# Kernel optimization log

Measured on AMD Instinct MI355X. Metric: run time of the kernel, lower is better.

The kernel has to match this reference:

```python
import jax, jax.numpy as jnp
import numpy as np

D_MODEL = 1024
N_HEADS = 16
D_K = D_MODEL // N_HEADS


def _xavier(key, shape):
    fan_in, fan_out = shape[1], shape[0]
    a = np.sqrt(6.0 / (fan_in + fan_out))
    return jax.random.uniform(key, shape, jnp.float32, -a, a)


def setup_inputs() -> dict:
    key = jax.random.key(0)
    kx, kq, kk, kv, ko = jax.random.split(key, 5)
    x = jax.random.normal(kx, (2, 2048, D_MODEL), jnp.float32)
    # nn.Linear weights are [out, in]; y = x @ W.T
    Wq = _xavier(kq, (D_MODEL, D_MODEL))
    Wk = _xavier(kk, (D_MODEL, D_MODEL))
    Wv = _xavier(kv, (D_MODEL, D_MODEL))
    Wo = _xavier(ko, (D_MODEL, D_MODEL))
    bo = jnp.zeros((D_MODEL,), jnp.float32)
    return {"x": x, "Wq": Wq, "Wk": Wk, "Wv": Wv, "Wo": Wo, "bo": bo}


def reference(x, Wq, Wk, Wv, Wo, bo):
    B, S, D = x.shape
    def split_heads(t):
        # [B,S,D] -> [B,H,S,d_k]
        return t.reshape(B, S, N_HEADS, D_K).transpose(0, 2, 1, 3)
    Q = split_heads(x @ Wq.T)
    K = split_heads(x @ Wk.T)
    V = split_heads(x @ Wv.T)
    scale = 1.0 / jnp.sqrt(jnp.asarray(D_K, x.dtype))
    scores = jnp.einsum('bhqd,bhkd->bhqk', Q, K) * scale  # [B,H,S,S]
    attn = jax.nn.softmax(scores, axis=-1)
    out = jnp.einsum('bhqk,bhkd->bhqd', attn, V)  # [B,H,S,d_k]
    out = out.transpose(0, 2, 1, 3).reshape(B, S, D)  # merge heads
    return out @ Wo.T + bo
```

## Files before the change

### kernel.cpp

```cpp
#include <hip/hip_runtime.h>


typedef __attribute__((ext_vector_type(8))) short bf16x8;
typedef __attribute__((ext_vector_type(4))) short bf16x4;
typedef __attribute__((ext_vector_type(4))) float f32x4;
typedef __attribute__((ext_vector_type(2))) unsigned int u32x2;

#define GK 1024
#define SEQ 2048
#define NHEAD 16
#define DKD 64
#define PADW 72

#define MFMA32(a, b, c) __builtin_amdgcn_mfma_f32_16x16x32_bf16((a), (b), (c), 0, 0, 0)

#if __has_builtin(__builtin_amdgcn_mfma_f32_16x16x16bf16_1k)
#define HAVE_MFMA16 1
#define MFMA16(a, b, c) __builtin_amdgcn_mfma_f32_16x16x16bf16_1k((a), (b), (c), 0, 0, 0)
#else
#define HAVE_MFMA16 0
#endif

#if __has_builtin(__builtin_amdgcn_exp2f)
#define EXP2(x) __builtin_amdgcn_exp2f(x)
#else
#define EXP2(x) exp2f(x)
#endif

#define QSCALE 0.18033688011f

static __device__ __forceinline__ unsigned short f2bf(float f) {
    unsigned int u = __float_as_uint(f);
    u += 0x7fffu + ((u >> 16) & 1u);
    return (unsigned short)(u >> 16);
}

static __device__ __forceinline__ unsigned int pack_bf2(float a, float b) {
    unsigned int ua = __float_as_uint(a) + 0x8000u;
    unsigned int ub = __float_as_uint(b) + 0x8000u;
    return __builtin_amdgcn_perm(ub, ua, 0x07060302u);
}

__global__ __launch_bounds__(256) void cast_all(const float* __restrict__ x,
                                                const float* __restrict__ wq,
                                                const float* __restrict__ wk,
                                                const float* __restrict__ wv,
                                                const float* __restrict__ wo,
                                                unsigned short* __restrict__ Xb,
                                                unsigned short* __restrict__ Wqkv,
                                                unsigned short* __restrict__ Wob) {
    const int bid = blockIdx.x;
    const float* src; unsigned short* dst; int off;
    if (bid < 4096)      { src = x;  dst = Xb;             off = bid; }
    else if (bid < 5120) { src = wq; dst = Wqkv;           off = bid - 4096; }
    else if (bid < 6144) { src = wk; dst = Wqkv + 1048576; off = bid - 5120; }
    else if (bid < 7168) { src = wv; dst = Wqkv + 2097152; off = bid - 6144; }
    else                 { src = wo; dst = Wob;            off = bid - 7168; }
    const int i = off * 1024 + threadIdx.x * 4;
    float4 v = *(const float4*)(src + i);
    u32x2 p; p.x = pack_bf2(v.x, v.y); p.y = pack_bf2(v.z, v.w);
    *(u32x2*)(dst + i) = p;
}

template <int MODE, int BN>
__global__ __launch_bounds__(256) void gemm_bt(const unsigned short* __restrict__ A,
                                               const unsigned short* __restrict__ Bw,
                                               unsigned short* __restrict__ outb,
                                               float* __restrict__ outf,
                                               const float* __restrict__ bias) {
    constexpr int NJ = BN / 32;
    __shared__ __align__(16) unsigned short As[128 * 32];
    __shared__ __align__(16) unsigned short Bs[BN * 32];
    __shared__ __align__(16) unsigned short E[(MODE == 0) ? 4 * 64 * PADW : 4];

    const int t    = threadIdx.x;
    const int lane = t & 63;
    const int w    = t >> 6;
    const int wm   = (w >> 1) * 64;
    const int wn   = (w & 1) * (BN / 2);
    const int bm0  = blockIdx.x * 128;
    const int bn0  = blockIdx.y * BN;
    const int lm   = lane & 15;
    const int lq   = lane >> 4;
    const int kc   = lq * 8;

    const unsigned short* Ab = A + (size_t)bm0 * GK;
    const unsigned short* Bb = Bw + (size_t)bn0 * GK;

    f32x4 acc[4][NJ];
#pragma unroll
    for (int i = 0; i < 4; i++)
#pragma unroll
        for (int j = 0; j < NJ; j++) acc[i][j] = (f32x4){0.f, 0.f, 0.f, 0.f};

    const int q_uni = (t & ~63);

    for (int k0 = 0; k0 < GK; k0 += 32) {
        __syncthreads();
#pragma unroll
        for (int i = 0; i < 2; ++i) {
            int q = i * 256 + t;
            int r = q >> 2;
            int c = (q & 3) * 8;
            int q0 = i * 256 + q_uni;
            __builtin_amdgcn_global_load_lds(
                (const __attribute__((address_space(1))) void*)(Ab + (size_t)r * GK + k0 + c),
                (__attribute__((address_space(3))) void*)(As + (size_t)q0 * 8),
                16, 0, 0);
        }
#pragma unroll
        for (int i = 0; i < BN / 64; ++i) {
            int q = i * 256 + t;
            int r = q >> 2;
            int c = (q & 3) * 8;
            int q0 = i * 256 + q_uni;
            __builtin_amdgcn_global_load_lds(
                (const __attribute__((address_space(1))) void*)(Bb + (size_t)r * GK + k0 + c),
                (__attribute__((address_space(3))) void*)(Bs + (size_t)q0 * 8),
                16, 0, 0);
        }
        __syncthreads();

        bf16x8 af[4], bf[NJ];
#pragma unroll
        for (int i = 0; i < 4; i++)
            af[i] = *(const bf16x8*)(As + (wm + i * 16 + lm) * 32 + kc);
#pragma unroll
        for (int j = 0; j < NJ; j++)
            bf[j] = *(const bf16x8*)(Bs + (wn + j * 16 + lm) * 32 + kc);
#pragma unroll
        for (int i = 0; i < 4; i++)
#pragma unroll
            for (int j = 0; j < NJ; j++)
                acc[i][j] = MFMA32(af[i], bf[j], acc[i][j]);
    }

    if (MODE == 0) {
        unsigned short* Ew = E + w * (64 * PADW);
        const int nbase = bn0 + wn;
        const int which = nbase >> 10;
        const int hh    = (nbase & 1023) >> 6;
        if (which != 2) {
            const float sc = (which == 0) ? QSCALE : 1.0f;
#pragma unroll
            for (int i = 0; i < 4; i++)
#pragma unroll
                for (int j = 0; j < 4; j++)
#pragma unroll
                    for (int r = 0; r < 4; r++)
                        Ew[(i * 16 + lq * 4 + r) * PADW + j * 16 + lm] =
                            f2bf(acc[i][j][r] * sc);
            unsigned short* dst = outb + (size_t)which * 4194304;
#pragma unroll
            for (int rep = 0; rep < 8; ++rep) {
                const int mm = rep * 8 + (lane >> 3);
                const int d0 = (lane & 7) * 8;
                uint4 v = *(const uint4*)(Ew + mm * PADW + d0);
                const int m_g = bm0 + wm + mm;
                const int b = m_g >> 11, s = m_g & 2047;
                *(uint4*)(dst + (((size_t)(b * NHEAD + hh)) * SEQ + s) * DKD + d0) = v;
            }
        } else {
#pragma unroll
            for (int i = 0; i < 4; i++)
#pragma unroll
                for (int j = 0; j < 4; j++) {
                    u32x2 pk;
                    pk.x = pack_bf2(acc[i][j][0], acc[i][j][1]);
                    pk.y = pack_bf2(acc[i][j][2], acc[i][j][3]);
                    *(u32x2*)(Ew + (j * 16 + lm) * PADW + i * 16 + lq * 4) = pk;
                }
            unsigned short* dst = outb + (size_t)2 * 4194304;
#pragma unroll
            for (int rep = 0; rep < 8; ++rep) {
                const int nn = rep * 8 + (lane >> 3);
                const int mc = (lane & 7) * 8;
                uint4 v = *(const uint4*)(Ew + nn * PADW + mc);
                const int m_g = bm0 + wm + mc;
                const int b = m_g >> 11, s0 = m_g & 2047;
                *(uint4*)(dst + (((size_t)(b * NHEAD + hh)) * DKD + nn) * SEQ + s0) = v;
            }
        }
    } else {
#pragma unroll
        for (int i = 0; i < 4; i++) {
            const int mbase = bm0 + wm + i * 16 + lq * 4;
#pragma unroll
            for (int j = 0; j < NJ; j++) {
                const int n = bn0 + wn + j * 16 + lm;
#pragma unroll
                for (int r = 0; r < 4; r++)
                    outf[(size_t)(mbase + r) * 1024 + n] = acc[i][j][r] + bias[n];
            }
        }
    }
}

__global__ __launch_bounds__(256) void attn_kernel(const unsigned short* __restrict__ Qg,
                                                   const unsigned short* __restrict__ Kg,
                                                   const unsigned short* __restrict__ Vtg,
                                                   unsigned short* __restrict__ Og) {
    __shared__ __align__(16) unsigned short KV[2][2][64 * PADW];
#if !HAVE_MFMA16
    __shared__ __align__(16) unsigned short Ps[128 * PADW];
#endif

    const int id  = blockIdx.x;
    const int xcd = id & 7;
    const int j8  = id >> 3;
    const int bh  = xcd * 4 + (j8 & 3);
    const int qb  = j8 >> 2;
    const unsigned short* Qp  = Qg  + ((size_t)bh * SEQ + qb * 128) * DKD;
    const unsigned short* Kp  = Kg  + (size_t)bh * SEQ * DKD;
    const unsigned short* Vtp = Vtg + (size_t)bh * DKD * SEQ;

    const int t    = threadIdx.x;
    const int lane = t & 63;
    const int w    = t >> 6;
    const int lm   = lane & 15;
    const int kq   = lane >> 4;
    const int qw   = w * 32;

    bf16x8 aq[2][2];
#pragma unroll
    for (int iq = 0; iq < 2; ++iq)
#pragma unroll
        for (int kk = 0; kk < 2; ++kk)
            aq[iq][kk] = *(const bf16x8*)(Qp + (size_t)(qw + iq * 16 + lm) * DKD + kk * 32 + kq * 8);

    f32x4 o[2][4];
    f32x4 ls[2];
#pragma unroll
    for (int iq = 0; iq < 2; ++iq) {
        ls[iq] = (f32x4){0.f, 0.f, 0.f, 0.f};
#pragma unroll
        for (int dj = 0; dj < 4; ++dj) o[iq][dj] = (f32x4){0.f, 0.f, 0.f, 0.f};
    }

    const int sr = t >> 2, sc = (t & 3) * 16;
    uint4 kreg0, kreg1, vreg0, vreg1;
    {
        const unsigned short* kp = Kp + (size_t)sr * DKD + sc;
        const unsigned short* vp = Vtp + (size_t)sr * SEQ + sc;
        uint4 a0 = *(const uint4*)(kp), a1 = *(const uint4*)(kp + 8);
        uint4 b0 = *(const uint4*)(vp), b1 = *(const uint4*)(vp + 8);
        uint4* dk = (uint4*)(&KV[0][0][sr * PADW + sc]); dk[0] = a0; dk[1] = a1;
        uint4* dv = (uint4*)(&KV[0][1][sr * PADW + sc]); dv[0] = b0; dv[1] = b1;
    }
    {
        const unsigned short* kp = Kp + (size_t)(64 + sr) * DKD + sc;
        kreg0 = *(const uint4*)(kp); kreg1 = *(const uint4*)(kp + 8);
        const unsigned short* vp = Vtp + (size_t)sr * SEQ + 64 + sc;
        vreg0 = *(const uint4*)(vp); vreg1 = *(const uint4*)(vp + 8);
    }

    for (int kt = 0; kt < 32; ++kt) {
        __syncthreads();
        if (kt + 1 < 32) {
            uint4* dk = (uint4*)(&KV[(kt + 1) & 1][0][sr * PADW + sc]);
            dk[0] = kreg0; dk[1] = kreg1;
            uint4* dv = (uint4*)(&KV[(kt + 1) & 1][1][sr * PADW + sc]);
            dv[0] = vreg0; dv[1] = vreg1;
        }
        if (kt + 2 < 32) {
            const unsigned short* kp = Kp + (size_t)((kt + 2) * 64 + sr) * DKD + sc;
            kreg0 = *(const uint4*)(kp); kreg1 = *(const uint4*)(kp + 8);
            const unsigned short* vp = Vtp + (size_t)sr * SEQ + (kt + 2) * 64 + sc;
            vreg0 = *(const uint4*)(vp); vreg1 = *(const uint4*)(vp + 8);
        }
        const unsigned short* Kc = &KV[kt & 1][0][0];
        const unsigned short* Vc = &KV[kt & 1][1][0];

        f32x4 s[4][2];
#pragma unroll
        for (int jk = 0; jk < 4; ++jk)
#pragma unroll
            for (int iq = 0; iq < 2; ++iq) s[jk][iq] = (f32x4){0.f, 0.f, 0.f, 0.f};
#pragma unroll
        for (int jk = 0; jk < 4; ++jk) {
            bf16x8 ak0 = *(const bf16x8*)(Kc + (jk * 16 + lm) * PADW + kq * 8);
            bf16x8 ak1 = *(const bf16x8*)(Kc + (jk * 16 + lm) * PADW + 32 + kq * 8);
#pragma unroll
            for (int iq = 0; iq < 2; ++iq) {
                s[jk][iq] = MFMA32(ak0, aq[iq][0], s[jk][iq]);
                s[jk][iq] = MFMA32(ak1, aq[iq][1], s[jk][iq]);
            }
        }

#pragma unroll
        for (int jk = 0; jk < 4; ++jk)
#pragma unroll
            for (int iq = 0; iq < 2; ++iq) {
#pragma unroll
                for (int r = 0; r < 4; ++r) s[jk][iq][r] = EXP2(s[jk][iq][r]);
                ls[iq] += s[jk][iq];
            }

#if HAVE_MFMA16
        bf16x4 ap[4][2];
#pragma unroll
        for (int jk = 0; jk < 4; ++jk)
#pragma unroll
            for (int iq = 0; iq < 2; ++iq) {
                u32x2 pk;
                pk.x = pack_bf2(s[jk][iq][0], s[jk][iq][1]);
                pk.y = pack_bf2(s[jk][iq][2], s[jk][iq][3]);
                ap[jk][iq] = __builtin_bit_cast(bf16x4, pk);
            }
#pragma unroll
        for (int jk = 0; jk < 4; ++jk)
#pragma unroll
            for (int dj = 0; dj < 4; ++dj) {
                bf16x4 bv = *(const bf16x4*)(Vc + (dj * 16 + lm) * PADW + jk * 16 + kq * 4);
#pragma unroll
                for (int iq = 0; iq < 2; ++iq)
                    o[iq][dj] = MFMA16(ap[jk][iq], bv, o[iq][dj]);
            }
#else
#pragma unroll
        for (int iq = 0; iq < 2; ++iq)
#pragma unroll
            for (int jk = 0; jk < 4; ++jk) {
                u32x2 pk;
                pk.x = pack_bf2(s[jk][iq][0], s[jk][iq][1]);
                pk.y = pack_bf2(s[jk][iq][2], s[jk][iq][3]);
                *(u32x2*)(Ps + (qw + iq * 16 + lm) * PADW + jk * 16 + kq * 4) = pk;
            }
        bf16x8 ap[2][2];
#pragma unroll
        for (int iq = 0; iq < 2; ++iq)
#pragma unroll
            for (int kk = 0; kk < 2; ++kk)
                ap[iq][kk] = *(const bf16x8*)(Ps + (qw + iq * 16 + lm) * PADW + kk * 32 + kq * 8);
#pragma unroll
        for (int dj = 0; dj < 4; ++dj) {
            bf16x8 bv0 = *(const bf16x8*)(Vc + (dj * 16 + lm) * PADW + kq * 8);
            bf16x8 bv1 = *(const bf16x8*)(Vc + (dj * 16 + lm) * PADW + 32 + kq * 8);
#pragma unroll
            for (int iq = 0; iq < 2; ++iq) {
                o[iq][dj] = MFMA32(ap[iq][0], bv0, o[iq][dj]);
                o[iq][dj] = MFMA32(ap[iq][1], bv1, o[iq][dj]);
            }
        }
#endif
    }

    const int b = bh >> 4, h = bh & 15;
    float linv[2];
#pragma unroll
    for (int iq = 0; iq < 2; ++iq) {
        float l = (ls[iq][0] + ls[iq][1]) + (ls[iq][2] + ls[iq][3]);
        l += __shfl_xor(l, 16);
        l += __shfl_xor(l, 32);
#if __has_builtin(__builtin_amdgcn_rcpf)
        linv[iq] = __builtin_amdgcn_rcpf(l);
#else
        linv[iq] = 1.0f / l;
#endif
    }
#pragma unroll
    for (int iq = 0; iq < 2; ++iq) {
#pragma unroll
        for (int r = 0; r < 4; ++r) {
            const float lv = __shfl(linv[iq], kq * 4 + r);
            const int qrow = qb * 128 + qw + iq * 16 + kq * 4 + r;
            unsigned short* op = Og + (((size_t)(b * SEQ + qrow)) * NHEAD + h) * DKD;
#pragma unroll
            for (int dj = 0; dj < 4; ++dj)
                op[dj * 16 + lm] = f2bf(o[iq][dj][r] * lv);
        }
    }
}

extern "C" void kernel_launch(void* const* d_in, const int* in_sizes, int n_in,
                              void* d_out, int out_size, void* d_ws, size_t ws_size,
                              hipStream_t stream) {
    const float* x  = (const float*)d_in[0];
    const float* Wq = (const float*)d_in[1];
    const float* Wk = (const float*)d_in[2];
    const float* Wv = (const float*)d_in[3];
    const float* Wo = (const float*)d_in[4];
    const float* bo = (const float*)d_in[5];
    float* out = (float*)d_out;

    unsigned short* ws = (unsigned short*)d_ws;
    unsigned short* Xb   = ws;
    unsigned short* Wqkv = ws + 4194304;
    unsigned short* Wob  = ws + 7340032;
    unsigned short* QKV  = ws + 8388608;
    unsigned short* Ob   = ws + 20971520;

    cast_all<<<8192, 256, 0, stream>>>(x, Wq, Wk, Wv, Wo, Xb, Wqkv, Wob);
    gemm_bt<0, 128><<<dim3(32, 24), 256, 0, stream>>>(Xb, Wqkv, QKV, nullptr, nullptr);
    attn_kernel<<<512, 256, 0, stream>>>(QKV, QKV + 4194304, QKV + 8388608, Ob);
    gemm_bt<1, 64><<<dim3(32, 16), 256, 0, stream>>>(Ob, Wob, nullptr, out, bo);
}
```

Measured before the change: 199.2 us.

## Split attention key tiles across waves and halve query tile per block

The attention kernel now handles 64 query rows per block instead of 128 and launches twice as many blocks. Each wave takes a 16-key slice of every 64-key tile for all 64 queries, rather than 32 queries against all keys. Partial outputs and row sums are combined across waves through shared memory at the end, which also gives vectorized 16-byte output stores. The goal is more blocks and occupancy (launch bounds 256,3) with less per-wave register state and fewer LDS K/V reads per query; the cost is the extra cross-wave reduction and more total K/V loading, since each tile is fetched by twice as many blocks.

```diff
diff --git a/kernel.cpp b/kernel.cpp
--- a/kernel.cpp
+++ b/kernel.cpp
@@ -13,13 +13,7 @@
 #define PADW 72
 
 #define MFMA32(a, b, c) __builtin_amdgcn_mfma_f32_16x16x32_bf16((a), (b), (c), 0, 0, 0)
-
-#if __has_builtin(__builtin_amdgcn_mfma_f32_16x16x16bf16_1k)
-#define HAVE_MFMA16 1
 #define MFMA16(a, b, c) __builtin_amdgcn_mfma_f32_16x16x16bf16_1k((a), (b), (c), 0, 0, 0)
-#else
-#define HAVE_MFMA16 0
-#endif
 
 #if __has_builtin(__builtin_amdgcn_exp2f)
 #define EXP2(x) __builtin_amdgcn_exp2f(x)
@@ -88,10 +82,11 @@
     const unsigned short* Bb = Bw + (size_t)bn0 * GK;
 
     f32x4 acc[4][NJ];
+    const f32x4 Z4 = {0.f, 0.f, 0.f, 0.f};
 #pragma unroll
     for (int i = 0; i < 4; i++)
 #pragma unroll
-        for (int j = 0; j < NJ; j++) acc[i][j] = (f32x4){0.f, 0.f, 0.f, 0.f};
+        for (int j = 0; j < NJ; j++) acc[i][j] = Z4;
 
     const int q_uni = (t & ~63);
 
@@ -196,21 +191,18 @@
     }
 }
 
-__global__ __launch_bounds__(256) void attn_kernel(const unsigned short* __restrict__ Qg,
-                                                   const unsigned short* __restrict__ Kg,
-                                                   const unsigned short* __restrict__ Vtg,
-                                                   unsigned short* __restrict__ Og) {
+__global__ __launch_bounds__(256, 3) void attn_kernel(const unsigned short* __restrict__ Qg,
+                                                      const unsigned short* __restrict__ Kg,
+                                                      const unsigned short* __restrict__ Vtg,
+                                                      unsigned short* __restrict__ Og) {
     __shared__ __align__(16) unsigned short KV[2][2][64 * PADW];
-#if !HAVE_MFMA16
-    __shared__ __align__(16) unsigned short Ps[128 * PADW];
-#endif
 
     const int id  = blockIdx.x;
     const int xcd = id & 7;
     const int j8  = id >> 3;
     const int bh  = xcd * 4 + (j8 & 3);
     const int qb  = j8 >> 2;
-    const unsigned short* Qp  = Qg  + ((size_t)bh * SEQ + qb * 128) * DKD;
+    const unsigned short* Qp  = Qg  + ((size_t)bh * SEQ + qb * 64) * DKD;
     const unsigned short* Kp  = Kg  + (size_t)bh * SEQ * DKD;
     const unsigned short* Vtp = Vtg + (size_t)bh * DKD * SEQ;
 
@@ -219,22 +211,23 @@
     const int w    = t >> 6;
     const int lm   = lane & 15;
     const int kq   = lane >> 4;
-    const int qw   = w * 32;
-
-    bf16x8 aq[2][2];
-#pragma unroll
-    for (int iq = 0; iq < 2; ++iq)
+
+    const f32x4 Z4 = {0.f, 0.f, 0.f, 0.f};
+
+    bf16x8 aq[4][2];
+#pragma unroll
+    for (int c = 0; c < 4; ++c)
 #pragma unroll
         for (int kk = 0; kk < 2; ++kk)
-            aq[iq][kk] = *(const bf16x8*)(Qp + (size_t)(qw + iq * 16 + lm) * DKD + kk * 32 + kq * 8);
-
-    f32x4 o[2][4];
-    f32x4 ls[2];
-#pragma unroll
-    for (int iq = 0; iq < 2; ++iq) {
-        ls[iq] = (f32x4){0.f, 0.f, 0.f, 0.f};
-#pragma unroll
-        for (int dj = 0; dj < 4; ++dj) o[iq][dj] = (f32x4){0.f, 0.f, 0.f, 0.f};
+            aq[c][kk] = *(const bf16x8*)(Qp + (size_t)(c * 16 + lm) * DKD + kk * 32 + kq * 8);
+
+    f32x4 o[4][4];
+    float ls[4];
+#pragma unroll
+    for (int c = 0; c < 4; ++c) {
+        ls[c] = 0.f;
+#pragma unroll
+        for (int dj = 0; dj < 4; ++dj) o[c][dj] = Z4;
     }
 
     const int sr = t >> 2, sc = (t & 3) * 16;
@@ -271,104 +264,88 @@
         const unsigned short* Kc = &KV[kt & 1][0][0];
         const unsigned short* Vc = &KV[kt & 1][1][0];
 
-        f32x4 s[4][2];
-#pragma unroll
-        for (int jk = 0; jk < 4; ++jk)
-#pragma unroll
-            for (int iq = 0; iq < 2; ++iq) s[jk][iq] = (f32x4){0.f, 0.f, 0.f, 0.f};
-#pragma unroll
-        for (int jk = 0; jk < 4; ++jk) {
-            bf16x8 ak0 = *(const bf16x8*)(Kc + (jk * 16 + lm) * PADW + kq * 8);
-            bf16x8 ak1 = *(const bf16x8*)(Kc + (jk * 16 + lm) * PADW + 32 + kq * 8);
-#pragma unroll
-            for (int iq = 0; iq < 2; ++iq) {
-                s[jk][iq] = MFMA32(ak0, aq[iq][0], s[jk][iq]);
-                s[jk][iq] = MFMA32(ak1, aq[iq][1], s[jk][iq]);
+        bf16x8 ak0 = *(const bf16x8*)(Kc + (w * 16 + lm) * PADW + kq * 8);
+        bf16x8 ak1 = *(const bf16x8*)(Kc + (w * 16 + lm) * PADW + 32 + kq * 8);
+        f32x4 s[4];
+#pragma unroll
+        for (int c = 0; c < 4; ++c) {
+            s[c] = MFMA32(ak0, aq[c][0], Z4);
+            s[c] = MFMA32(ak1, aq[c][1], s[c]);
+        }
+
+#pragma unroll
+        for (int c = 0; c < 4; ++c) {
+#pragma unroll
+            for (int r = 0; r < 4; ++r) s[c][r] = EXP2(s[c][r]);
+            ls[c] += (s[c][0] + s[c][1]) + (s[c][2] + s[c][3]);
+        }
+
+        bf16x4 ap[4];
+#pragma unroll
+        for (int c = 0; c < 4; ++c) {
+            u32x2 pk;
+            pk.x = pack_bf2(s[c][0], s[c][1]);
+            pk.y = pack_bf2(s[c][2], s[c][3]);
+            ap[c] = __builtin_bit_cast(bf16x4, pk);
+        }
+
+#pragma unroll
+        for (int dj = 0; dj < 4; ++dj) {
+            bf16x4 bv = *(const bf16x4*)(Vc + (dj * 16 + lm) * PADW + w * 16 + kq * 4);
+#pragma unroll
+            for (int c = 0; c < 4; ++c)
+                o[c][dj] = MFMA16(ap[c], bv, o[c][dj]);
+        }
+    }
+
+    __syncthreads();
+    float* Lf = (float*)(&KV[0][0][0]);
+
+#pragma unroll
+    for (int c = 0; c < 4; ++c) {
+        float v = ls[c];
+        v += __shfl_xor(v, 16);
+        v += __shfl_xor(v, 32);
+        if (kq == 0) Lf[w * 64 + c * 16 + lm] = v;
+    }
+    __syncthreads();
+
+    const int rq = t >> 2;
+    const int dq = (t & 3) * 8;
+    float li = (Lf[rq] + Lf[64 + rq]) + (Lf[128 + rq] + Lf[192 + rq]);
+#if __has_builtin(__builtin_amdgcn_rcpf)
+    li = __builtin_amdgcn_rcpf(li);
+#else
+    li = 1.0f / li;
+#endif
+    __syncthreads();
+
+    const int b = bh >> 4, h = bh & 15;
+#pragma unroll
+    for (int p = 0; p < 2; ++p) {
+#pragma unroll
+        for (int c = 0; c < 4; ++c)
+#pragma unroll
+            for (int djh = 0; djh < 2; ++djh) {
+                const int dj = 2 * p + djh;
+#pragma unroll
+                for (int r = 0; r < 4; ++r)
+                    Lf[(w * 64 + c * 16 + kq * 4 + r) * 36 + djh * 16 + lm] = o[c][dj][r];
             }
-        }
-
-#pragma unroll
-        for (int jk = 0; jk < 4; ++jk)
-#pragma unroll
-            for (int iq = 0; iq < 2; ++iq) {
-#pragma unroll
-                for (int r = 0; r < 4; ++r) s[jk][iq][r] = EXP2(s[jk][iq][r]);
-                ls[iq] += s[jk][iq];
-            }
-
-#if HAVE_MFMA16
-        bf16x4 ap[4][2];
-#pragma unroll
-        for (int jk = 0; jk < 4; ++jk)
-#pragma unroll
-            for (int iq = 0; iq < 2; ++iq) {
-                u32x2 pk;
-                pk.x = pack_bf2(s[jk][iq][0], s[jk][iq][1]);
-                pk.y = pack_bf2(s[jk][iq][2], s[jk][iq][3]);
-                ap[jk][iq] = __builtin_bit_cast(bf16x4, pk);
-            }
-#pragma unroll
-        for (int jk = 0; jk < 4; ++jk)
-#pragma unroll
-            for (int dj = 0; dj < 4; ++dj) {
-                bf16x4 bv = *(const bf16x4*)(Vc + (dj * 16 + lm) * PADW + jk * 16 + kq * 4);
-#pragma unroll
-                for (int iq = 0; iq < 2; ++iq)
-                    o[iq][dj] = MFMA16(ap[jk][iq], bv, o[iq][dj]);
-            }
-#else
-#pragma unroll
-        for (int iq = 0; iq < 2; ++iq)
-#pragma unroll
-            for (int jk = 0; jk < 4; ++jk) {
-                u32x2 pk;
-                pk.x = pack_bf2(s[jk][iq][0], s[jk][iq][1]);
-                pk.y = pack_bf2(s[jk][iq][2], s[jk][iq][3]);
-                *(u32x2*)(Ps + (qw + iq * 16 + lm) * PADW + jk * 16 + kq * 4) = pk;
-            }
-        bf16x8 ap[2][2];
-#pragma unroll
-        for (int iq = 0; iq < 2; ++iq)
-#pragma unroll
-            for (int kk = 0; kk < 2; ++kk)
-                ap[iq][kk] = *(const bf16x8*)(Ps + (qw + iq * 16 + lm) * PADW + kk * 32 + kq * 8);
-#pragma unroll
-        for (int dj = 0; dj < 4; ++dj) {
-            bf16x8 bv0 = *(const bf16x8*)(Vc + (dj * 16 + lm) * PADW + kq * 8);
-            bf16x8 bv1 = *(const bf16x8*)(Vc + (dj * 16 + lm) * PADW + 32 + kq * 8);
-#pragma unroll
-            for (int iq = 0; iq < 2; ++iq) {
-                o[iq][dj] = MFMA32(ap[iq][0], bv0, o[iq][dj]);
-                o[iq][dj] = MFMA32(ap[iq][1], bv1, o[iq][dj]);
-            }
-        }
-#endif
-    }
-
-    const int b = bh >> 4, h = bh & 15;
-    float linv[2];
-#pragma unroll
-    for (int iq = 0; iq < 2; ++iq) {
-        float l = (ls[iq][0] + ls[iq][1]) + (ls[iq][2] + ls[iq][3]);
-        l += __shfl_xor(l, 16);
-        l += __shfl_xor(l, 32);
-#if __has_builtin(__builtin_amdgcn_rcpf)
-        linv[iq] = __builtin_amdgcn_rcpf(l);
-#else
-        linv[iq] = 1.0f / l;
-#endif
-    }
-#pragma unroll
-    for (int iq = 0; iq < 2; ++iq) {
-#pragma unroll
-        for (int r = 0; r < 4; ++r) {
-            const float lv = __shfl(linv[iq], kq * 4 + r);
-            const int qrow = qb * 128 + qw + iq * 16 + kq * 4 + r;
-            unsigned short* op = Og + (((size_t)(b * SEQ + qrow)) * NHEAD + h) * DKD;
-#pragma unroll
-            for (int dj = 0; dj < 4; ++dj)
-                op[dj * 16 + lm] = f2bf(o[iq][dj][r] * lv);
-        }
+        __syncthreads();
+        f32x4 a0 = Z4, a1 = Z4;
+#pragma unroll
+        for (int wp = 0; wp < 4; ++wp) {
+            a0 += *(const f32x4*)(Lf + (wp * 64 + rq) * 36 + dq);
+            a1 += *(const f32x4*)(Lf + (wp * 64 + rq) * 36 + dq + 4);
+        }
+        uint4 outv;
+        outv.x = pack_bf2(a0[0] * li, a0[1] * li);
+        outv.y = pack_bf2(a0[2] * li, a0[3] * li);
+        outv.z = pack_bf2(a1[0] * li, a1[1] * li);
+        outv.w = pack_bf2(a1[2] * li, a1[3] * li);
+        *(uint4*)(Og + (((size_t)(b * SEQ + qb * 64 + rq)) * NHEAD + h) * DKD + p * 32 + dq) = outv;
+        __syncthreads();
     }
 }
 
@@ -392,6 +369,6 @@
 
     cast_all<<<8192, 256, 0, stream>>>(x, Wq, Wk, Wv, Wo, Xb, Wqkv, Wob);
     gemm_bt<0, 128><<<dim3(32, 24), 256, 0, stream>>>(Xb, Wqkv, QKV, nullptr, nullptr);
-    attn_kernel<<<512, 256, 0, stream>>>(QKV, QKV + 4194304, QKV + 8388608, Ob);
+    attn_kernel<<<1024, 256, 0, stream>>>(QKV, QKV + 4194304, QKV + 8388608, Ob);
     gemm_bt<1, 64><<<dim3(32, 16), 256, 0, stream>>>(Ob, Wob, nullptr, out, bo);
 }
```

After: 197.9 us. Within noise of the previous version (-0.6%).
